# Kernel tuning notes

Hardware: AMD Instinct MI355X
Metric: run time of the kernel (lower is better)

Reference implementation:

```python
import jax, jax.numpy as jnp
import numpy as np

B, S, E, H, ML = 4, 1024, 1024, 16, 2048
HD = E // H


def setup_inputs() -> dict:
    key = jax.random.key(0)
    ks = jax.random.split(key, 8)
    s = 0.02
    return {
        "x": jax.random.normal(ks[0], (B, S, E), dtype=jnp.float32),
        "rel_pos": jax.random.normal(ks[1], (H, ML), dtype=jnp.float32),
        "in_proj_w": jax.random.normal(ks[2], (3 * E, E), dtype=jnp.float32) * s,
        "in_proj_b": jnp.zeros((3 * E,), jnp.float32),
        "out_w": jax.random.normal(ks[3], (E, E), dtype=jnp.float32) * s,
        "out_b": jnp.zeros((E,), jnp.float32),
        "w1": jax.random.normal(ks[4], (4 * E, E), dtype=jnp.float32) * s,
        "b1": jnp.zeros((4 * E,), jnp.float32),
        "w2": jax.random.normal(ks[5], (E, 4 * E), dtype=jnp.float32) * s,
        "b2": jnp.zeros((E,), jnp.float32),
        "ln1_g": jnp.ones((E,), jnp.float32),
        "ln1_b": jnp.zeros((E,), jnp.float32),
        "ln2_g": jnp.ones((E,), jnp.float32),
        "ln2_b": jnp.zeros((E,), jnp.float32),
    }


def _layernorm(x, g, b, eps=1e-5):
    m = x.mean(-1, keepdims=True)
    v = ((x - m) ** 2).mean(-1, keepdims=True)
    return (x - m) * jax.lax.rsqrt(v + eps) * g + b


def _causal_mask(size, rel_pos):
    # rel_pos: [H, max_len]; size <= max_len branch of the torch code
    flipped = jnp.flip(rel_pos[:, :size], -1)                        # [H, size]
    neg_inf = jnp.full((rel_pos.shape[0], size), -jnp.inf, rel_pos.dtype)
    padded = jnp.concatenate([flipped, neg_inf], axis=-1)            # [H, 2*size]
    idx = jnp.arange(size)[None, :] - jnp.arange(size)[:, None] + size - 1
    return padded[:, idx]                                            # [H, S, S]: rel_pos[i-j] if j<=i else -inf


def reference(x, rel_pos, in_proj_w, in_proj_b, out_w, out_b,
              w1, b1, w2, b2, ln1_g, ln1_b, ln2_g, ln2_b):
    b, s, e = x.shape
    xn = _layernorm(x, ln1_g, ln1_b)
    qkv = xn @ in_proj_w.T + in_proj_b                               # [B,S,3E]
    q, k, v = jnp.split(qkv, 3, axis=-1)
    q = q.reshape(b, s, H, HD).transpose(0, 2, 1, 3)                 # [B,H,S,D]
    k = k.reshape(b, s, H, HD).transpose(0, 2, 1, 3)
    v = v.reshape(b, s, H, HD).transpose(0, 2, 1, 3)
    mask = _causal_mask(s, rel_pos)                                  # [H,S,S], broadcast over batch (== repeat(B,1,1))
    scores = jnp.einsum("bhqd,bhkd->bhqk", q, k) / np.sqrt(HD) + mask[None]
    attn = jax.nn.softmax(scores, axis=-1)
    o = jnp.einsum("bhqk,bhkd->bhqd", attn, v)                       # [B,H,S,D]
    o = o.transpose(0, 2, 1, 3).reshape(b, s, e)
    att_out = o @ out_w.T + out_b
    x = x + att_out
    xm = _layernorm(x, ln2_g, ln2_b)
    mlp = jax.nn.relu(xm @ w1.T + b1) @ w2.T + b2
    return x + mlp
```

## Files before the change

kernel.cpp:

```cpp
#include <hip/hip_runtime.h>
#include <stdint.h>

typedef __bf16 bf16x8 __attribute__((ext_vector_type(8)));
typedef float  f32x4  __attribute__((ext_vector_type(4)));

__device__ __forceinline__ unsigned short f2bf(float f) {
  union { float f; unsigned int u; } a; a.f = f;
  unsigned int r = a.u + 0x7FFFu + ((a.u >> 16) & 1u);
  return (unsigned short)(r >> 16);
}

__device__ __forceinline__ unsigned short f2bf_fast(float f) {
  union { __bf16 b; unsigned short u; } v; v.b = (__bf16)f; return v.u;
}

__device__ __forceinline__ void cp16(const void* g, void* l) {
  auto g1 = reinterpret_cast<__attribute__((address_space(1))) unsigned int*>(
      reinterpret_cast<uintptr_t>(g));
  auto l3 = reinterpret_cast<__attribute__((address_space(3))) unsigned int*>(
      reinterpret_cast<uintptr_t>(l));
  __builtin_amdgcn_global_load_lds(g1, l3, 16, 0, 0);
}

__global__ __launch_bounds__(256) void cvt_ln1(
    const float* __restrict__ s0, const float* __restrict__ s1,
    const float* __restrict__ s2, const float* __restrict__ s3,
    unsigned short* __restrict__ d0, unsigned short* __restrict__ d1,
    unsigned short* __restrict__ d2, unsigned short* __restrict__ d3,
    const float* __restrict__ x,
    const float* __restrict__ g,
    const float* __restrict__ bta,
    unsigned short* __restrict__ out) {
  if (blockIdx.x < 12288) {
    int i = (blockIdx.x * 256 + threadIdx.x) * 4;
    const float* src; unsigned short* dst; int off;
    if (i < 3145728)       { src = s0; dst = d0; off = 0; }
    else if (i < 4194304)  { src = s1; dst = d1; off = 3145728; }
    else if (i < 8388608)  { src = s2; dst = d2; off = 4194304; }
    else                   { src = s3; dst = d3; off = 8388608; }
    i -= off;
    float4 v = *(const float4*)(src + i);
    union { unsigned short u[4]; uint2 p; } o;
    o.u[0] = f2bf(v.x); o.u[1] = f2bf(v.y); o.u[2] = f2bf(v.z); o.u[3] = f2bf(v.w);
    *(uint2*)(dst + i) = o.p;
    return;
  }
  const int row = blockIdx.x - 12288, t = threadIdx.x;
  const float4 v = *(const float4*)(x + (size_t)row * 1024 + t * 4);
  float s1v = v.x + v.y + v.z + v.w;
  float s2v = v.x*v.x + v.y*v.y + v.z*v.z + v.w*v.w;
  #pragma unroll
  for (int off = 1; off < 64; off <<= 1) {
    s1v += __shfl_xor(s1v, off, 64);
    s2v += __shfl_xor(s2v, off, 64);
  }
  __shared__ float r1[4], r2[4];
  if ((t & 63) == 0) { r1[t >> 6] = s1v; r2[t >> 6] = s2v; }
  __syncthreads();
  s1v = r1[0] + r1[1] + r1[2] + r1[3];
  s2v = r2[0] + r2[1] + r2[2] + r2[3];
  const float mean = s1v * (1.0f / 1024.0f);
  const float var  = s2v * (1.0f / 1024.0f) - mean * mean;
  const float rstd = rsqrtf(var + 1e-5f);
  const float4 gv = *(const float4*)(g + t * 4);
  const float4 bv = *(const float4*)(bta + t * 4);
  union { unsigned short u[4]; uint2 p; } o;
  o.u[0] = f2bf((v.x - mean) * rstd * gv.x + bv.x);
  o.u[1] = f2bf((v.y - mean) * rstd * gv.y + bv.y);
  o.u[2] = f2bf((v.z - mean) * rstd * gv.z + bv.z);
  o.u[3] = f2bf((v.w - mean) * rstd * gv.w + bv.w);
  *(uint2*)(out + (size_t)row * 1024 + t * 4) = o.p;
}

__global__ __launch_bounds__(256) void fold_ln(
    const float* __restrict__ x,
    const float* __restrict__ P0,
    const float* __restrict__ P1,
    const float* __restrict__ ob_bias,
    const float* __restrict__ g,
    const float* __restrict__ bta,
    unsigned short* __restrict__ out,
    const float* __restrict__ seed_bias,
    float* __restrict__ seed_out) {
  const int row = blockIdx.x, t = threadIdx.x;
  const size_t off = (size_t)row * 1024 + t * 4;
  float4 v = *(const float4*)(x + off);
  const float4 p0 = *(const float4*)(P0 + off);
  const float4 p1 = *(const float4*)(P1 + off);
  const float4 ob = *(const float4*)(ob_bias + t * 4);
  v.x += p0.x + p1.x + ob.x;
  v.y += p0.y + p1.y + ob.y;
  v.z += p0.z + p1.z + ob.z;
  v.w += p0.w + p1.w + ob.w;
  {
    float4 sb = *(const float4*)(seed_bias + t * 4);
    float4 sv;
    sv.x = v.x + sb.x; sv.y = v.y + sb.y; sv.z = v.z + sb.z; sv.w = v.w + sb.w;
    *(float4*)(seed_out + off) = sv;
  }
  float s1 = v.x + v.y + v.z + v.w;
  float s2 = v.x*v.x + v.y*v.y + v.z*v.z + v.w*v.w;
  #pragma unroll
  for (int o2 = 1; o2 < 64; o2 <<= 1) {
    s1 += __shfl_xor(s1, o2, 64);
    s2 += __shfl_xor(s2, o2, 64);
  }
  __shared__ float r1[4], r2[4];
  if ((t & 63) == 0) { r1[t >> 6] = s1; r2[t >> 6] = s2; }
  __syncthreads();
  s1 = r1[0] + r1[1] + r1[2] + r1[3];
  s2 = r2[0] + r2[1] + r2[2] + r2[3];
  const float mean = s1 * (1.0f / 1024.0f);
  const float var  = s2 * (1.0f / 1024.0f) - mean * mean;
  const float rstd = rsqrtf(var + 1e-5f);
  const float4 gv = *(const float4*)(g + t * 4);
  const float4 bv = *(const float4*)(bta + t * 4);
  union { unsigned short u[4]; uint2 p; } o;
  o.u[0] = f2bf((v.x - mean) * rstd * gv.x + bv.x);
  o.u[1] = f2bf((v.y - mean) * rstd * gv.y + bv.y);
  o.u[2] = f2bf((v.z - mean) * rstd * gv.z + bv.z);
  o.u[3] = f2bf((v.w - mean) * rstd * gv.w + bv.w);
  *(uint2*)(out + off) = o.p;
}

template <int MODE>
__device__ __forceinline__ void gemm_core(
    const unsigned short* __restrict__ A,
    const unsigned short* __restrict__ Bt,
    const float* __restrict__ bias,
    void* __restrict__ outp,
    int N, int K, int kbeg, int kend,
    unsigned short* As, unsigned short* Bs) {
  const int tid = threadIdx.x;
  const int wave = tid >> 6, lane = tid & 63;
  const int q = lane >> 4, c = lane & 15;
  const int wm = (wave & 1) << 6, wn = (wave >> 1) << 6;
  const int m0 = blockIdx.x << 7, n0 = blockIdx.y << 7;

  const int srow = tid >> 3;
  const int cg8  = ((tid & 7) ^ (srow & 7)) << 3;

  const unsigned short* gA = A  + (size_t)(m0 + srow) * K + cg8;
  const unsigned short* gB = Bt + (size_t)(n0 + srow) * K + cg8;
  const size_t rstep = (size_t)32 * K;

  auto issue = [&](int k0, int buf) {
    unsigned short* lA = As + buf * 8192 + tid * 8;
    unsigned short* lB = Bs + buf * 8192 + tid * 8;
    #pragma unroll
    for (int it = 0; it < 4; it++) {
      cp16(gA + it * rstep + k0, lA + it * 2048);
      cp16(gB + it * rstep + k0, lB + it * 2048);
    }
  };

  const f32x4 fzero = {0.f, 0.f, 0.f, 0.f};
  f32x4 acc[4][4];
  #pragma unroll
  for (int i = 0; i < 4; i++)
    #pragma unroll
    for (int j = 0; j < 4; j++) acc[i][j] = fzero;

  issue(kbeg, 0);
  if (kbeg + 64 < kend) issue(kbeg + 64, 1);

  int buf = 0;
  for (int k0 = kbeg; k0 < kend; k0 += 64, buf ^= 1) {
    if (k0 + 64 < kend) asm volatile("s_waitcnt vmcnt(8)" ::: "memory");
    else                asm volatile("s_waitcnt vmcnt(0)" ::: "memory");
    asm volatile("s_barrier" ::: "memory");

    const unsigned short* cA = As + buf * 8192;
    const unsigned short* cB = Bs + buf * 8192;
    #pragma unroll
    for (int ks = 0; ks < 2; ks++) {
      const int sw = (((ks << 2) + q) ^ (c & 7)) << 3;
      bf16x8 af[4], bf[4];
      #pragma unroll
      for (int i = 0; i < 4; i++) af[i] = *(const bf16x8*)&cA[(wm + i*16 + c)*64 + sw];
      #pragma unroll
      for (int j = 0; j < 4; j++) bf[j] = *(const bf16x8*)&cB[(wn + j*16 + c)*64 + sw];
      #pragma unroll
      for (int i = 0; i < 4; i++)
        #pragma unroll
        for (int j = 0; j < 4; j++)
          acc[i][j] = __builtin_amdgcn_mfma_f32_16x16x32_bf16(af[i], bf[j], acc[i][j], 0, 0, 0);
    }

    asm volatile("s_barrier" ::: "memory");
    if (k0 + 128 < kend) issue(k0 + 128, buf);
  }

  if (MODE == 5) {
    float* op = (float*)outp;
    #pragma unroll
    for (int i = 0; i < 4; i++) {
      #pragma unroll
      for (int r = 0; r < 4; r++) {
        const int row = m0 + wm + i * 16 + q * 4 + r;
        #pragma unroll
        for (int j = 0; j < 4; j++) {
          const int col = n0 + wn + j * 16 + c;
          op[(size_t)row * N + col] = acc[i][j][r];
        }
      }
    }
  } else {
    float bj[4];
    #pragma unroll
    for (int j = 0; j < 4; j++) bj[j] = bias[n0 + wn + j * 16 + c];
    #pragma unroll
    for (int i = 0; i < 4; i++) {
      #pragma unroll
      for (int r = 0; r < 4; r++) {
        const int row = m0 + wm + i * 16 + q * 4 + r;
        #pragma unroll
        for (int j = 0; j < 4; j++) {
          const int col = n0 + wn + j * 16 + c;
          const size_t idx = (size_t)row * N + col;
          float v = acc[i][j][r] + bj[j];
          if (MODE == 0) ((unsigned short*)outp)[idx] = f2bf(v);
          else           ((unsigned short*)outp)[idx] = f2bf(fmaxf(v, 0.f));
        }
      }
    }
  }
}

template <int MODE>
__global__ __launch_bounds__(256, 2) void gemm_bt(
    const unsigned short* __restrict__ A,
    const unsigned short* __restrict__ Bt,
    const float* __restrict__ bias,
    void* __restrict__ outp,
    int N, int K) {
  __shared__ __align__(16) unsigned short As[2 * 8192];
  __shared__ __align__(16) unsigned short Bs[2 * 8192];
  gemm_core<MODE>(A, Bt, bias, outp, N, K, 0, K, As, Bs);
}

__global__ __launch_bounds__(256, 2) void gemm_bt_splitk_p(
    const unsigned short* __restrict__ A,
    const unsigned short* __restrict__ Bt,
    float* __restrict__ Q0,
    float* __restrict__ Q1,
    int N, int K) {
  __shared__ __align__(16) unsigned short As[2 * 8192];
  __shared__ __align__(16) unsigned short Bs[2 * 8192];
  const int KH = K >> 1;
  const int kbeg = blockIdx.z * KH;
  gemm_core<5>(A, Bt, nullptr, blockIdx.z ? Q1 : Q0, N, K, kbeg, kbeg + KH, As, Bs);
}

__global__ __launch_bounds__(256) void fold2(
    const float* __restrict__ Q0,
    const float* __restrict__ Q1,
    float* __restrict__ out) {
  int i = (blockIdx.x * 256 + threadIdx.x) * 4;
  #pragma unroll
  for (int it = 0; it < 2; it++) {
    float4 a  = *(const float4*)(out + i);
    float4 q0 = *(const float4*)(Q0 + i);
    float4 q1 = *(const float4*)(Q1 + i);
    a.x += q0.x + q1.x; a.y += q0.y + q1.y;
    a.z += q0.z + q1.z; a.w += q0.w + q1.w;
    *(float4*)(out + i) = a;
    i += 2097152;
  }
}

__global__ __launch_bounds__(256, 2) void attn_flash(
    const unsigned short* __restrict__ qkv,
    const float* __restrict__ rel_pos,
    unsigned short* __restrict__ o) {
  __shared__ __align__(16) unsigned short Qs[128 * 64];
  __shared__ __align__(16) unsigned short Ks[2][64 * 64];
  __shared__ __align__(16) unsigned short Vs[2][64 * 64];
  __shared__ __align__(16) unsigned short Ps[4][32 * 64];
  __shared__ float rps[1024];

  const int tid = threadIdx.x;
  const int wave = tid >> 6, lane = tid & 63;
  const int q = lane >> 4, c = lane & 15;

  const int lid = blockIdx.x + (blockIdx.y << 3);
  const int xq = lid & 7, y = lid >> 3;
  const int qt = (y & 32) ? (7 - xq) : xq;
  const int b = y >> 4, h = y & 15;

  const unsigned short* qg = qkv + (size_t)b * 1024 * 3072 + h * 64;
  const unsigned short* kg = qg + 1024;
  const unsigned short* vg = qg + 2048;

  #pragma unroll
  for (int i = 0; i < 4; i++) {
    const int idx = tid + i * 256;
    rps[idx & 1023] = rel_pos[h * 2048 + (idx & 1023)] * 1.44269504f;
  }

  const int sr  = tid >> 3;
  const int cg8 = ((tid & 7) ^ (sr & 7)) << 3;
  #pragma unroll
  for (int it = 0; it < 4; it++)
    cp16(qg + (size_t)(qt * 128 + sr + it * 32) * 3072 + cg8, &Qs[(tid + it * 256) * 8]);

  const int vrow = tid & 63, d0 = (tid >> 6) << 4;
  const int vchunk = vrow >> 3, vlo = vrow & 7;

  cp16(kg + (size_t)sr * 3072 + cg8, &Ks[0][tid * 8]);
  cp16(kg + (size_t)(sr + 32) * 3072 + cg8, &Ks[0][(tid + 256) * 8]);
  union { int4 v; unsigned short u[8]; } va, vb2;
  {
    const unsigned short* vrp = vg + (size_t)vrow * 3072 + d0;
    va.v  = *(const int4*)vrp;
    vb2.v = *(const int4*)(vrp + 8);
  }
  __syncthreads();

  bf16x8 qf[2][2];
  #pragma unroll
  for (int mt = 0; mt < 2; mt++)
    #pragma unroll
    for (int ks = 0; ks < 2; ks++)
      qf[mt][ks] = *(const bf16x8*)&Qs[(wave*32 + mt*16 + c)*64 + ((((ks<<2)+q) ^ (c & 7)) << 3)];

  const f32x4 fzero = {0.f, 0.f, 0.f, 0.f};
  f32x4 O[2][4];
  float l_i[2][4];
  #pragma unroll
  for (int mt = 0; mt < 2; mt++) {
    #pragma unroll
    for (int r = 0; r < 4; r++) l_i[mt][r] = 0.f;
    #pragma unroll
    for (int dt = 0; dt < 4; dt++) O[mt][dt] = fzero;
  }

  unsigned short* Pw = &Ps[wave][0];
  const int i_base = qt * 128 + wave * 32;

  const float sc = 0.125f * 1.44269504f;
  const int kdiag = qt << 1;
  const int nkt = (qt + 1) * 2;

  for (int kt = 0; kt < nkt; kt++) {
    const int buf = kt & 1;

    asm volatile("s_waitcnt vmcnt(0)" ::: "memory");

    #pragma unroll
    for (int j = 0; j < 8; j++) {
      const int pos = ((vchunk ^ j) << 3) + vlo;
      Vs[buf][(d0 + j) * 64 + pos]     = va.u[j];
      Vs[buf][(d0 + 8 + j) * 64 + pos] = vb2.u[j];
    }

    __syncthreads();

    if (kt + 1 < nkt) {
      cp16(kg + (size_t)((kt + 1) * 64 + sr) * 3072 + cg8, &Ks[buf ^ 1][tid * 8]);
      cp16(kg + (size_t)((kt + 1) * 64 + sr + 32) * 3072 + cg8, &Ks[buf ^ 1][(tid + 256) * 8]);
      const unsigned short* vrp = vg + (size_t)((kt + 1) * 64 + vrow) * 3072 + d0;
      va.v  = *(const int4*)vrp;
      vb2.v = *(const int4*)(vrp + 8);
    }

    f32x4 S[2][4];
    #pragma unroll
    for (int mt = 0; mt < 2; mt++)
      #pragma unroll
      for (int nt = 0; nt < 4; nt++) S[mt][nt] = fzero;
    #pragma unroll
    for (int ks = 0; ks < 2; ks++) {
      const int sw = (((ks << 2) + q) ^ (c & 7)) << 3;
      bf16x8 kb[4];
      #pragma unroll
      for (int nt = 0; nt < 4; nt++) kb[nt] = *(const bf16x8*)&Ks[buf][(nt*16 + c)*64 + sw];
      #pragma unroll
      for (int mt = 0; mt < 2; mt++)
        #pragma unroll
        for (int nt = 0; nt < 4; nt++)
          S[mt][nt] = __builtin_amdgcn_mfma_f32_16x16x32_bf16(qf[mt][ks], kb[nt], S[mt][nt], 0, 0, 0);
    }

    if (kt < kdiag) {
      #pragma unroll
      for (int mt = 0; mt < 2; mt++) {
        #pragma unroll
        for (int r = 0; r < 4; r++) {
          const int i_ = i_base + mt * 16 + q * 4 + r;
          const int prow = (mt * 16 + q * 4 + r) * 64;
          const int rsw  = (q * 4 + r) & 7;
          float s = 0.f;
          #pragma unroll
          for (int nt = 0; nt < 4; nt++) {
            const int j_ = kt * 64 + nt * 16 + c;
            const float p = exp2f(fmaf(S[mt][nt][r], sc, rps[i_ - j_]));
            s += p;
            Pw[prow + ((((nt << 1) + (c >> 3)) ^ rsw) << 3) + (c & 7)] = f2bf_fast(p);
          }
          l_i[mt][r] += s;
        }
      }
    } else {
      #pragma unroll
      for (int mt = 0; mt < 2; mt++) {
        #pragma unroll
        for (int r = 0; r < 4; r++) {
          const int i_ = i_base + mt * 16 + q * 4 + r;
          const int prow = (mt * 16 + q * 4 + r) * 64;
          const int rsw  = (q * 4 + r) & 7;
          float s = 0.f;
          #pragma unroll
          for (int nt = 0; nt < 4; nt++) {
            const int j_ = kt * 64 + nt * 16 + c;
            const int d_ = i_ - j_;
            const float p = (d_ >= 0)
                ? exp2f(fmaf(S[mt][nt][r], sc, rps[d_ & 1023])) : 0.f;
            s += p;
            Pw[prow + ((((nt << 1) + (c >> 3)) ^ rsw) << 3) + (c & 7)] = f2bf_fast(p);
          }
          l_i[mt][r] += s;
        }
      }
    }

    asm volatile("s_waitcnt lgkmcnt(0)" ::: "memory");

    #pragma unroll
    for (int ks = 0; ks < 2; ks++) {
      const int sw = (((ks << 2) + q) ^ (c & 7)) << 3;
      bf16x8 pa[2], vb[4];
      #pragma unroll
      for (int mt = 0; mt < 2; mt++) pa[mt] = *(const bf16x8*)&Pw[(mt*16 + c)*64 + sw];
      #pragma unroll
      for (int dt = 0; dt < 4; dt++) vb[dt] = *(const bf16x8*)&Vs[buf][(dt*16 + c)*64 + sw];
      #pragma unroll
      for (int mt = 0; mt < 2; mt++)
        #pragma unroll
        for (int dt = 0; dt < 4; dt++)
          O[mt][dt] = __builtin_amdgcn_mfma_f32_16x16x32_bf16(pa[mt], vb[dt], O[mt][dt], 0, 0, 0);
    }
  }

  #pragma unroll
  for (int mt = 0; mt < 2; mt++) {
    #pragma unroll
    for (int r = 0; r < 4; r++) {
      float l = l_i[mt][r];
      l += __shfl_xor(l, 1, 64);
      l += __shfl_xor(l, 2, 64);
      l += __shfl_xor(l, 4, 64);
      l += __shfl_xor(l, 8, 64);
      const float inv = 1.0f / l;
      const int i_ = i_base + mt * 16 + q * 4 + r;
      unsigned short* orow = o + (size_t)(b * 1024 + i_) * 1024 + h * 64 + c;
      #pragma unroll
      for (int dt = 0; dt < 4; dt++) orow[dt * 16] = f2bf(O[mt][dt][r] * inv);
    }
  }
}

extern "C" void kernel_launch(void* const* d_in, const int* in_sizes, int n_in,
                              void* d_out, int out_size, void* d_ws, size_t ws_size,
                              hipStream_t stream) {
  (void)in_sizes; (void)n_in; (void)out_size; (void)ws_size;
  const float* x    = (const float*)d_in[0];
  const float* rel  = (const float*)d_in[1];
  const float* ipw  = (const float*)d_in[2];
  const float* ipb  = (const float*)d_in[3];
  const float* outw = (const float*)d_in[4];
  const float* outb = (const float*)d_in[5];
  const float* w1   = (const float*)d_in[6];
  const float* b1   = (const float*)d_in[7];
  const float* w2   = (const float*)d_in[8];
  const float* b2   = (const float*)d_in[9];
  const float* ln1g = (const float*)d_in[10];
  const float* ln1b = (const float*)d_in[11];
  const float* ln2g = (const float*)d_in[12];
  const float* ln2b = (const float*)d_in[13];

  unsigned short* ipw_b  = (unsigned short*)d_ws;
  unsigned short* outw_b = ipw_b  + (size_t)3072 * 1024;
  unsigned short* w1_b   = outw_b + (size_t)1024 * 1024;
  unsigned short* w2_b   = w1_b   + (size_t)4096 * 1024;
  unsigned short* xn     = w2_b   + (size_t)1024 * 4096;
  unsigned short* qkvb   = xn     + (size_t)4096 * 1024;
  unsigned short* ob     = qkvb   + (size_t)4096 * 3072;
  unsigned short* hb     = qkvb;
  unsigned short* xm     = xn;
  float*          x2     = (float*)(ob + (size_t)4096 * 1024);
  float*          P0     = (float*)qkvb;
  float*          P1     = x2;
  float*          Q0     = (float*)d_ws;
  float*          Q1     = x2;

  cvt_ln1<<<16384, 256, 0, stream>>>(ipw, outw, w1, w2, ipw_b, outw_b, w1_b, w2_b,
                                     x, ln1g, ln1b, xn);

  gemm_bt<0><<<dim3(32, 24), 256, 0, stream>>>(xn, ipw_b, ipb, qkvb, 3072, 1024);

  attn_flash<<<dim3(8, 64), 256, 0, stream>>>(qkvb, rel, ob);

  gemm_bt_splitk_p<<<dim3(32, 8, 2), 256, 0, stream>>>(ob, outw_b, P0, P1, 1024, 1024);

  fold_ln<<<4096, 256, 0, stream>>>(x, P0, P1, outb, ln2g, ln2b, xm, b2, (float*)d_out);

  gemm_bt<2><<<dim3(32, 32), 256, 0, stream>>>(xm, w1_b, b1, hb, 4096, 1024);

  gemm_bt_splitk_p<<<dim3(32, 8, 2), 256, 0, stream>>>(hb, w2_b, Q0, Q1, 1024, 4096);
  fold2<<<2048, 256, 0, stream>>>(Q0, Q1, (float*)d_out);
}
```

Measured before the change: 306.3 us.

## Overlap weight conversion with QKV GEMM, swizzle tile order, prioritize MFMA waves

Only the in_proj weight is now converted alongside LN1. The out_w, w1 and w2 conversions move into extra blocks of the QKV GEMM launch so they run concurrently with it. GEMM blocks get an XCD-aware tile remap that groups nearby output tiles to improve L2 reuse on the QKV and split-K GEMMs. The attention kernel raises wave priority around its MFMA sections. The conversion blocks compete with GEMM blocks for CUs, and the swizzle formula assumes specific grid shapes.

Result: slower. 315.0 us (+2.8%).

```diff
diff --git a/kernel.cpp b/kernel.cpp
--- a/kernel.cpp
+++ b/kernel.cpp
@@ -22,30 +22,25 @@
   __builtin_amdgcn_global_load_lds(g1, l3, 16, 0, 0);
 }
 
+__device__ __forceinline__ void cvt4(const float* src, unsigned short* dst, int i) {
+  float4 v = *(const float4*)(src + i);
+  union { unsigned short u[4]; uint2 p; } o;
+  o.u[0] = f2bf(v.x); o.u[1] = f2bf(v.y); o.u[2] = f2bf(v.z); o.u[3] = f2bf(v.w);
+  *(uint2*)(dst + i) = o.p;
+}
+
 __global__ __launch_bounds__(256) void cvt_ln1(
-    const float* __restrict__ s0, const float* __restrict__ s1,
-    const float* __restrict__ s2, const float* __restrict__ s3,
-    unsigned short* __restrict__ d0, unsigned short* __restrict__ d1,
-    unsigned short* __restrict__ d2, unsigned short* __restrict__ d3,
+    const float* __restrict__ s0,
+    unsigned short* __restrict__ d0,
     const float* __restrict__ x,
     const float* __restrict__ g,
     const float* __restrict__ bta,
     unsigned short* __restrict__ out) {
-  if (blockIdx.x < 12288) {
-    int i = (blockIdx.x * 256 + threadIdx.x) * 4;
-    const float* src; unsigned short* dst; int off;
-    if (i < 3145728)       { src = s0; dst = d0; off = 0; }
-    else if (i < 4194304)  { src = s1; dst = d1; off = 3145728; }
-    else if (i < 8388608)  { src = s2; dst = d2; off = 4194304; }
-    else                   { src = s3; dst = d3; off = 8388608; }
-    i -= off;
-    float4 v = *(const float4*)(src + i);
-    union { unsigned short u[4]; uint2 p; } o;
-    o.u[0] = f2bf(v.x); o.u[1] = f2bf(v.y); o.u[2] = f2bf(v.z); o.u[3] = f2bf(v.w);
-    *(uint2*)(dst + i) = o.p;
+  if (blockIdx.x < 3072) {
+    cvt4(s0, d0, (blockIdx.x * 256 + threadIdx.x) * 4);
     return;
   }
-  const int row = blockIdx.x - 12288, t = threadIdx.x;
+  const int row = blockIdx.x - 3072, t = threadIdx.x;
   const float4 v = *(const float4*)(x + (size_t)row * 1024 + t * 4);
   float s1v = v.x + v.y + v.z + v.w;
   float s2v = v.x*v.x + v.y*v.y + v.z*v.z + v.w*v.w;
@@ -123,19 +118,30 @@
   *(uint2*)(out + off) = o.p;
 }
 
-template <int MODE>
+template <int MODE, int SWZ>
 __device__ __forceinline__ void gemm_core(
     const unsigned short* __restrict__ A,
     const unsigned short* __restrict__ Bt,
     const float* __restrict__ bias,
     void* __restrict__ outp,
     int N, int K, int kbeg, int kend,
-    unsigned short* As, unsigned short* Bs) {
+    unsigned short* As, unsigned short* Bs,
+    int bid, int nwg) {
   const int tid = threadIdx.x;
   const int wave = tid >> 6, lane = tid & 63;
   const int q = lane >> 4, c = lane & 15;
   const int wm = (wave & 1) << 6, wn = (wave >> 1) << 6;
-  const int m0 = blockIdx.x << 7, n0 = blockIdx.y << 7;
+
+  int m0, n0;
+  if (SWZ) {
+    const int v_ = (bid & 7) * (nwg >> 3) + (bid >> 3);
+    const int patch = v_ >> 6, u_ = v_ & 63;
+    m0 = (((patch & 3) << 3) + (u_ & 7)) << 7;
+    n0 = (((patch >> 2) << 3) + (u_ >> 3)) << 7;
+  } else {
+    m0 = (bid & 31) << 7;
+    n0 = (bid >> 5) << 7;
+  }
 
   const int srow = tid >> 3;
   const int cg8  = ((tid & 7) ^ (srow & 7)) << 3;
@@ -227,7 +233,7 @@
   }
 }
 
-template <int MODE>
+template <int MODE, int SWZ>
 __global__ __launch_bounds__(256, 2) void gemm_bt(
     const unsigned short* __restrict__ A,
     const unsigned short* __restrict__ Bt,
@@ -236,7 +242,31 @@
     int N, int K) {
   __shared__ __align__(16) unsigned short As[2 * 8192];
   __shared__ __align__(16) unsigned short Bs[2 * 8192];
-  gemm_core<MODE>(A, Bt, bias, outp, N, K, 0, K, As, Bs);
+  gemm_core<MODE, SWZ>(A, Bt, bias, outp, N, K, 0, K, As, Bs,
+                       blockIdx.x + (blockIdx.y << 5), gridDim.x * gridDim.y);
+}
+
+__global__ __launch_bounds__(256, 2) void qkv_cvt(
+    const unsigned short* __restrict__ A,
+    const unsigned short* __restrict__ Bt,
+    const float* __restrict__ bias,
+    unsigned short* __restrict__ outp,
+    const float* __restrict__ cw0, unsigned short* __restrict__ cd0,
+    const float* __restrict__ cw1, unsigned short* __restrict__ cd1,
+    const float* __restrict__ cw2, unsigned short* __restrict__ cd2) {
+  if (blockIdx.x >= 768) {
+    int b = blockIdx.x - 768;
+    const float* src; unsigned short* dst;
+    if (b < 1024)      { src = cw0; dst = cd0; }
+    else if (b < 5120) { src = cw1; dst = cd1; b -= 1024; }
+    else               { src = cw2; dst = cd2; b -= 5120; }
+    cvt4(src, dst, (b * 256 + threadIdx.x) * 4);
+    return;
+  }
+  __shared__ __align__(16) unsigned short As[2 * 8192];
+  __shared__ __align__(16) unsigned short Bs[2 * 8192];
+  gemm_core<0, 1>(A, Bt, bias, outp, 3072, 1024, 0, 1024, As, Bs,
+                  blockIdx.x, 768);
 }
 
 __global__ __launch_bounds__(256, 2) void gemm_bt_splitk_p(
@@ -249,7 +279,8 @@
   __shared__ __align__(16) unsigned short Bs[2 * 8192];
   const int KH = K >> 1;
   const int kbeg = blockIdx.z * KH;
-  gemm_core<5>(A, Bt, nullptr, blockIdx.z ? Q1 : Q0, N, K, kbeg, kbeg + KH, As, Bs);
+  gemm_core<5, 1>(A, Bt, nullptr, blockIdx.z ? Q1 : Q0, N, K, kbeg, kbeg + KH,
+                  As, Bs, blockIdx.x + (blockIdx.y << 5), gridDim.x * gridDim.y);
 }
 
 __global__ __launch_bounds__(256) void fold2(
@@ -369,6 +400,7 @@
     for (int mt = 0; mt < 2; mt++)
       #pragma unroll
       for (int nt = 0; nt < 4; nt++) S[mt][nt] = fzero;
+    __builtin_amdgcn_s_setprio(1);
     #pragma unroll
     for (int ks = 0; ks < 2; ks++) {
       const int sw = (((ks << 2) + q) ^ (c & 7)) << 3;
@@ -381,6 +413,7 @@
         for (int nt = 0; nt < 4; nt++)
           S[mt][nt] = __builtin_amdgcn_mfma_f32_16x16x32_bf16(qf[mt][ks], kb[nt], S[mt][nt], 0, 0, 0);
     }
+    __builtin_amdgcn_s_setprio(0);
 
     if (kt < kdiag) {
       #pragma unroll
@@ -426,6 +459,7 @@
 
     asm volatile("s_waitcnt lgkmcnt(0)" ::: "memory");
 
+    __builtin_amdgcn_s_setprio(1);
     #pragma unroll
     for (int ks = 0; ks < 2; ks++) {
       const int sw = (((ks << 2) + q) ^ (c & 7)) << 3;
@@ -440,6 +474,7 @@
         for (int dt = 0; dt < 4; dt++)
           O[mt][dt] = __builtin_amdgcn_mfma_f32_16x16x32_bf16(pa[mt], vb[dt], O[mt][dt], 0, 0, 0);
     }
+    __builtin_amdgcn_s_setprio(0);
   }
 
   #pragma unroll
@@ -494,10 +529,10 @@
   float*          Q0     = (float*)d_ws;
   float*          Q1     = x2;
 
-  cvt_ln1<<<16384, 256, 0, stream>>>(ipw, outw, w1, w2, ipw_b, outw_b, w1_b, w2_b,
-                                     x, ln1g, ln1b, xn);
-
-  gemm_bt<0><<<dim3(32, 24), 256, 0, stream>>>(xn, ipw_b, ipb, qkvb, 3072, 1024);
+  cvt_ln1<<<7168, 256, 0, stream>>>(ipw, ipw_b, x, ln1g, ln1b, xn);
+
+  qkv_cvt<<<9984, 256, 0, stream>>>(xn, ipw_b, ipb, qkvb,
+                                    outw, outw_b, w1, w1_b, w2, w2_b);
 
   attn_flash<<<dim3(8, 64), 256, 0, stream>>>(qkvb, rel, ob);
 
@@ -505,7 +540,7 @@
 
   fold_ln<<<4096, 256, 0, stream>>>(x, P0, P1, outb, ln2g, ln2b, xm, b2, (float*)d_out);
 
-  gemm_bt<2><<<dim3(32, 32), 256, 0, stream>>>(xm, w1_b, b1, hb, 4096, 1024);
+  gemm_bt<2, 0><<<dim3(32, 32), 256, 0, stream>>>(xm, w1_b, b1, hb, 4096, 1024);
 
   gemm_bt_splitk_p<<<dim3(32, 8, 2), 256, 0, stream>>>(hb, w2_b, Q0, Q1, 1024, 4096);
   fold2<<<2048, 256, 0, stream>>>(Q0, Q1, (float*)d_out);
```
